# Performance work log

Measured on AMD Instinct MI355X. Metric: run time of the kernel, lower is better.

Reference implementation:

```python
import jax, jax.numpy as jnp
import numpy as np

B = 65536      # batch (edges/nodes)
A = 8          # number of attribute node types (len(cfg.node_types))
E = 128        # embedding_size


def setup_inputs() -> dict:
    key = jax.random.key(0)
    k1, k2, k3, k4, k5 = jax.random.split(key, 5)
    image_features = jax.random.normal(k1, (B, E), dtype=jnp.float32)
    edge_attributes = jax.random.normal(k2, (B, A, E), dtype=jnp.float32)
    # nn.Linear(2E -> E): weight [E, 2E], bias [E]
    W_agg = jax.random.normal(k3, (E, 2 * E), dtype=jnp.float32) * (1.0 / np.sqrt(2 * E))
    b_agg = jax.random.normal(k4, (E,), dtype=jnp.float32) * 0.01
    # per-node-type edge-space projection [A, E, E] (kaiming-uniform-like scale)
    proj = jax.random.uniform(k5, (A, E, E), dtype=jnp.float32, minval=-1.0, maxval=1.0) * np.sqrt(6.0 / E)
    return {
        "image_features": image_features,
        "edge_attributes": edge_attributes,
        "W_agg": W_agg,
        "b_agg": b_agg,
        "proj": proj,
    }


def reference(image_features, edge_attributes, W_agg, b_agg, proj):
    # src_embeddings.unsqueeze(1).repeat(1, A, 1) -> broadcast, no copy
    src = jnp.broadcast_to(image_features[:, None, :], edge_attributes.shape)  # [B, A, E]
    x = jnp.concatenate([src, edge_attributes], axis=-1)                       # [B, A, 2E]
    agg = jnp.einsum('bak,ik->bai', x, W_agg) + b_agg                          # Linear(2E->E)
    out = jnp.einsum('bai,aij->baj', agg, proj)                                # per-type matmul
    return out
```

## Files before the change

kernel.cpp:

```cpp
#include <hip/hip_runtime.h>
#include <hip/hip_bf16.h>

typedef __attribute__((ext_vector_type(8))) short short8;
typedef __attribute__((ext_vector_type(4))) float floatx4;

__device__ inline short f2bf(float f) {
  unsigned u = __builtin_bit_cast(unsigned, f);
  unsigned r = u + 0x7fffu + ((u >> 16) & 1u);
  return (short)(r >> 16);
}

__device__ inline short8 cvt8(float4 a, float4 b) {
  short8 r;
  r[0] = f2bf(a.x); r[1] = f2bf(a.y); r[2] = f2bf(a.z); r[3] = f2bf(a.w);
  r[4] = f2bf(b.x); r[5] = f2bf(b.y); r[6] = f2bf(b.z); r[7] = f2bf(b.w);
  return r;
}

__global__ __launch_bounds__(256) void prep_M(
    const float* __restrict__ W, const float* __restrict__ proj,
    const float* __restrict__ bvec, short* __restrict__ Mt,
    float* __restrict__ bias2) {
  int blk = blockIdx.x;
  int a = blk >> 7, j = blk & 127;
  int k = threadIdx.x;
  const float* pj = proj + a * 16384 + j;
  float acc = 0.f;
#pragma unroll 4
  for (int i = 0; i < 128; ++i)
    acc += W[i * 256 + k] * pj[i * 128];
  Mt[a * 32768 + j * 256 + k] = f2bf(acc);
  if (k == 0) {
    float b = 0.f;
    for (int i = 0; i < 128; ++i) b += bvec[i] * pj[i * 128];
    bias2[a * 128 + j] = b;
  }
}

__global__ __launch_bounds__(256) void gemm_main(
    const float* __restrict__ img, const float* __restrict__ edge,
    const short* __restrict__ Mt, const float* __restrict__ bias2,
    float* __restrict__ out) {
  constexpr int LDA = 40;
  __shared__ short As[128 * LDA];
  __shared__ short Bs[128 * LDA];

  const int tid = threadIdx.x;
  const int a = blockIdx.x & 7;
  const int b0 = (blockIdx.x >> 3) << 7;
  const int wave = tid >> 6, lane = tid & 63;
  const int quad = lane >> 4, l16 = lane & 15;
  const int wm = wave & 1, wn = wave >> 1;

  floatx4 acc[4][4] = {};
  const short* Mta = Mt + a * 32768;

  for (int ks = 0; ks < 8; ++ks) {
#pragma unroll
    for (int i = 0; i < 2; ++i) {
      int slot = tid + i * 256;
      int row = slot >> 2, c8 = slot & 3;
      const float* src;
      if (ks < 4)
        src = img + (size_t)(b0 + row) * 128 + ks * 32 + c8 * 8;
      else
        src = edge + (size_t)(b0 + row) * 1024 + a * 128 + (ks - 4) * 32 + c8 * 8;
      float4 v0 = *(const float4*)src;
      float4 v1 = *(const float4*)(src + 4);
      *(short8*)&As[row * LDA + c8 * 8] = cvt8(v0, v1);
    }
#pragma unroll
    for (int i = 0; i < 2; ++i) {
      int chunk = tid + i * 256;
      int row = chunk >> 2, c = chunk & 3;
      *(short8*)&Bs[row * LDA + c * 8] =
          *(const short8*)(Mta + row * 256 + ks * 32 + c * 8);
    }
    __syncthreads();

    short8 af[4], bfr[4];
#pragma unroll
    for (int mt = 0; mt < 4; ++mt)
      af[mt] = *(const short8*)&As[(wm * 64 + mt * 16 + l16) * LDA + quad * 8];
#pragma unroll
    for (int nt = 0; nt < 4; ++nt)
      bfr[nt] = *(const short8*)&Bs[(wn * 64 + nt * 16 + l16) * LDA + quad * 8];
#pragma unroll
    for (int mt = 0; mt < 4; ++mt)
#pragma unroll
      for (int nt = 0; nt < 4; ++nt)
        acc[mt][nt] = __builtin_amdgcn_mfma_f32_16x16x32_bf16(
            af[mt], bfr[nt], acc[mt][nt], 0, 0, 0);
    __syncthreads();
  }

  float bias[4];
#pragma unroll
  for (int nt = 0; nt < 4; ++nt)
    bias[nt] = bias2[a * 128 + wn * 64 + nt * 16 + l16];
#pragma unroll
  for (int mt = 0; mt < 4; ++mt)
#pragma unroll
    for (int nt = 0; nt < 4; ++nt) {
      int j = wn * 64 + nt * 16 + l16;
#pragma unroll
      for (int r = 0; r < 4; ++r) {
        int b = b0 + wm * 64 + mt * 16 + quad * 4 + r;
        out[(size_t)b * 1024 + a * 128 + j] = acc[mt][nt][r] + bias[nt];
      }
    }
}

extern "C" void kernel_launch(void* const* d_in, const int* in_sizes, int n_in,
                              void* d_out, int out_size, void* d_ws,
                              size_t ws_size, hipStream_t stream) {
  const float* img  = (const float*)d_in[0];
  const float* edge = (const float*)d_in[1];
  const float* W    = (const float*)d_in[2];
  const float* bv   = (const float*)d_in[3];
  const float* proj = (const float*)d_in[4];
  float* out = (float*)d_out;

  short* Mt = (short*)d_ws;
  float* bias2 = (float*)((char*)d_ws + 8 * 128 * 256 * 2);

  prep_M<<<1024, 256, 0, stream>>>(W, proj, bv, Mt, bias2);
  gemm_main<<<4096, 256, 0, stream>>>(img, edge, Mt, bias2, out);
}
```

Before: 508.5 us.

## Load MFMA fragments directly from global memory, dropping LDS staging and barriers

```diff
diff --git a/kernel.cpp b/kernel.cpp
--- a/kernel.cpp
+++ b/kernel.cpp
@@ -37,14 +37,10 @@
   }
 }
 
-__global__ __launch_bounds__(256) void gemm_main(
+__global__ __launch_bounds__(256, 3) void gemm_main(
     const float* __restrict__ img, const float* __restrict__ edge,
     const short* __restrict__ Mt, const float* __restrict__ bias2,
     float* __restrict__ out) {
-  constexpr int LDA = 40;
-  __shared__ short As[128 * LDA];
-  __shared__ short Bs[128 * LDA];
-
   const int tid = threadIdx.x;
   const int a = blockIdx.x & 7;
   const int b0 = (blockIdx.x >> 3) << 7;
@@ -53,45 +49,46 @@
   const int wm = wave & 1, wn = wave >> 1;
 
   floatx4 acc[4][4] = {};
+
+  const float* imgB[4];
+  const float* edgeB[4];
+  const short* mB[4];
+#pragma unroll
+  for (int mt = 0; mt < 4; ++mt) {
+    int row = b0 + wm * 64 + mt * 16 + l16;
+    imgB[mt]  = img  + (size_t)row * 128  + quad * 8;
+    edgeB[mt] = edge + (size_t)row * 1024 + a * 128 + quad * 8;
+  }
   const short* Mta = Mt + a * 32768;
+#pragma unroll
+  for (int nt = 0; nt < 4; ++nt)
+    mB[nt] = Mta + (wn * 64 + nt * 16 + l16) * 256 + quad * 8;
 
+#pragma unroll
   for (int ks = 0; ks < 8; ++ks) {
+    float4 v0[4], v1[4];
+    short8 bfr[4];
 #pragma unroll
-    for (int i = 0; i < 2; ++i) {
-      int slot = tid + i * 256;
-      int row = slot >> 2, c8 = slot & 3;
-      const float* src;
-      if (ks < 4)
-        src = img + (size_t)(b0 + row) * 128 + ks * 32 + c8 * 8;
-      else
-        src = edge + (size_t)(b0 + row) * 1024 + a * 128 + (ks - 4) * 32 + c8 * 8;
-      float4 v0 = *(const float4*)src;
-      float4 v1 = *(const float4*)(src + 4);
-      *(short8*)&As[row * LDA + c8 * 8] = cvt8(v0, v1);
+    for (int mt = 0; mt < 4; ++mt) {
+      const float* s = (ks < 4) ? (imgB[mt] + ks * 32)
+                                : (edgeB[mt] + (ks - 4) * 32);
+      v0[mt] = *(const float4*)s;
+      v1[mt] = *(const float4*)(s + 4);
     }
 #pragma unroll
-    for (int i = 0; i < 2; ++i) {
-      int chunk = tid + i * 256;
-      int row = chunk >> 2, c = chunk & 3;
-      *(short8*)&Bs[row * LDA + c * 8] =
-          *(const short8*)(Mta + row * 256 + ks * 32 + c * 8);
-    }
-    __syncthreads();
+    for (int nt = 0; nt < 4; ++nt)
+      bfr[nt] = *(const short8*)(mB[nt] + ks * 32);
 
-    short8 af[4], bfr[4];
+    short8 af[4];
 #pragma unroll
-    for (int mt = 0; mt < 4; ++mt)
-      af[mt] = *(const short8*)&As[(wm * 64 + mt * 16 + l16) * LDA + quad * 8];
-#pragma unroll
-    for (int nt = 0; nt < 4; ++nt)
-      bfr[nt] = *(const short8*)&Bs[(wn * 64 + nt * 16 + l16) * LDA + quad * 8];
+    for (int mt = 0; mt < 4; ++mt) af[mt] = cvt8(v0[mt], v1[mt]);
+
 #pragma unroll
     for (int mt = 0; mt < 4; ++mt)
 #pragma unroll
       for (int nt = 0; nt < 4; ++nt)
         acc[mt][nt] = __builtin_amdgcn_mfma_f32_16x16x32_bf16(
             af[mt], bfr[nt], acc[mt][nt], 0, 0, 0);
-    __syncthreads();
   }
 
   float bias[4];
```

Measured after the change: 615.8 us. 1.21x slower.

## Restructure GEMM to 16-row tiles covering all types, B read from global

Applied to the files above, without the earlier changes.

```diff
diff --git a/kernel.cpp b/kernel.cpp
--- a/kernel.cpp
+++ b/kernel.cpp
@@ -1,7 +1,7 @@
 #include <hip/hip_runtime.h>
-#include <hip/hip_bf16.h>
 
 typedef __attribute__((ext_vector_type(8))) short short8;
+typedef __attribute__((ext_vector_type(4))) short bfx4;
 typedef __attribute__((ext_vector_type(4))) float floatx4;
 
 __device__ inline short f2bf(float f) {
@@ -10,10 +10,9 @@
   return (short)(r >> 16);
 }
 
-__device__ inline short8 cvt8(float4 a, float4 b) {
-  short8 r;
+__device__ inline bfx4 cvt4(float4 a) {
+  bfx4 r;
   r[0] = f2bf(a.x); r[1] = f2bf(a.y); r[2] = f2bf(a.z); r[3] = f2bf(a.w);
-  r[4] = f2bf(b.x); r[5] = f2bf(b.y); r[6] = f2bf(b.z); r[7] = f2bf(b.w);
   return r;
 }
 
@@ -29,7 +28,9 @@
 #pragma unroll 4
   for (int i = 0; i < 128; ++i)
     acc += W[i * 256 + k] * pj[i * 128];
-  Mt[a * 32768 + j * 256 + k] = f2bf(acc);
+  int ks = k >> 5, quad = (k >> 3) & 3, e = k & 7;
+  int nt = j >> 4, l16 = j & 15;
+  Mt[((a * 8 + ks) * 8 + nt) * 512 + l16 * 32 + quad * 8 + e] = f2bf(acc);
   if (k == 0) {
     float b = 0.f;
     for (int i = 0; i < 128; ++i) b += bvec[i] * pj[i * 128];
@@ -37,78 +38,60 @@
   }
 }
 
-__global__ __launch_bounds__(256) void gemm_main(
+__global__ __launch_bounds__(512, 4) void gemm_main(
     const float* __restrict__ img, const float* __restrict__ edge,
     const short* __restrict__ Mt, const float* __restrict__ bias2,
     float* __restrict__ out) {
-  constexpr int LDA = 40;
-  __shared__ short As[128 * LDA];
-  __shared__ short Bs[128 * LDA];
+  __shared__ short imgS[16 * 136];
+  __shared__ short edgeS[16 * 1032];
 
   const int tid = threadIdx.x;
-  const int a = blockIdx.x & 7;
-  const int b0 = (blockIdx.x >> 3) << 7;
-  const int wave = tid >> 6, lane = tid & 63;
+  const int b0 = blockIdx.x << 4;
+  const int wave = tid >> 6;
+  const int lane = tid & 63;
   const int quad = lane >> 4, l16 = lane & 15;
-  const int wm = wave & 1, wn = wave >> 1;
 
-  floatx4 acc[4][4] = {};
-  const short* Mta = Mt + a * 32768;
+  float4 vi = *(const float4*)(img + (size_t)(b0 + (tid >> 5)) * 128 + (tid & 31) * 4);
+  float4 ve[8];
+#pragma unroll
+  for (int i = 0; i < 8; ++i) {
+    int f = i * 512 + tid;
+    ve[i] = *(const float4*)(edge + (size_t)(b0 + (f >> 8)) * 1024 + (f & 255) * 4);
+  }
+  *(bfx4*)((char*)imgS + (tid >> 5) * 272 + (tid & 31) * 8) = cvt4(vi);
+#pragma unroll
+  for (int i = 0; i < 8; ++i) {
+    int f = i * 512 + tid;
+    *(bfx4*)((char*)edgeS + (f >> 8) * 2064 + (f & 255) * 8) = cvt4(ve[i]);
+  }
+  __syncthreads();
 
+  const short* mB = Mt + wave * 32768 + l16 * 32 + quad * 8;
+  floatx4 acc[8] = {};
+#pragma unroll
   for (int ks = 0; ks < 8; ++ks) {
+    short8 af;
+    if (ks < 4)
+      af = *(const short8*)((const char*)imgS + l16 * 272 + (ks * 32 + quad * 8) * 2);
+    else
+      af = *(const short8*)((const char*)edgeS +
+                            l16 * 2064 + (wave * 128 + (ks - 4) * 32 + quad * 8) * 2);
 #pragma unroll
-    for (int i = 0; i < 2; ++i) {
-      int slot = tid + i * 256;
-      int row = slot >> 2, c8 = slot & 3;
-      const float* src;
-      if (ks < 4)
-        src = img + (size_t)(b0 + row) * 128 + ks * 32 + c8 * 8;
-      else
-        src = edge + (size_t)(b0 + row) * 1024 + a * 128 + (ks - 4) * 32 + c8 * 8;
-      float4 v0 = *(const float4*)src;
-      float4 v1 = *(const float4*)(src + 4);
-      *(short8*)&As[row * LDA + c8 * 8] = cvt8(v0, v1);
+    for (int nt = 0; nt < 8; ++nt) {
+      short8 bf = *(const short8*)(mB + ks * 4096 + nt * 512);
+      acc[nt] = __builtin_amdgcn_mfma_f32_16x16x32_bf16(af, bf, acc[nt], 0, 0, 0);
     }
-#pragma unroll
-    for (int i = 0; i < 2; ++i) {
-      int chunk = tid + i * 256;
-      int row = chunk >> 2, c = chunk & 3;
-      *(short8*)&Bs[row * LDA + c * 8] =
-          *(const short8*)(Mta + row * 256 + ks * 32 + c * 8);
-    }
-    __syncthreads();
-
-    short8 af[4], bfr[4];
-#pragma unroll
-    for (int mt = 0; mt < 4; ++mt)
-      af[mt] = *(const short8*)&As[(wm * 64 + mt * 16 + l16) * LDA + quad * 8];
-#pragma unroll
-    for (int nt = 0; nt < 4; ++nt)
-      bfr[nt] = *(const short8*)&Bs[(wn * 64 + nt * 16 + l16) * LDA + quad * 8];
-#pragma unroll
-    for (int mt = 0; mt < 4; ++mt)
-#pragma unroll
-      for (int nt = 0; nt < 4; ++nt)
-        acc[mt][nt] = __builtin_amdgcn_mfma_f32_16x16x32_bf16(
-            af[mt], bfr[nt], acc[mt][nt], 0, 0, 0);
-    __syncthreads();
   }
 
-  float bias[4];
+  float bias[8];
 #pragma unroll
-  for (int nt = 0; nt < 4; ++nt)
-    bias[nt] = bias2[a * 128 + wn * 64 + nt * 16 + l16];
+  for (int nt = 0; nt < 8; ++nt) bias[nt] = bias2[wave * 128 + nt * 16 + l16];
+  float* ob = out + (size_t)b0 * 1024 + wave * 128 + l16;
 #pragma unroll
-  for (int mt = 0; mt < 4; ++mt)
+  for (int nt = 0; nt < 8; ++nt)
 #pragma unroll
-    for (int nt = 0; nt < 4; ++nt) {
-      int j = wn * 64 + nt * 16 + l16;
-#pragma unroll
-      for (int r = 0; r < 4; ++r) {
-        int b = b0 + wm * 64 + mt * 16 + quad * 4 + r;
-        out[(size_t)b * 1024 + a * 128 + j] = acc[mt][nt][r] + bias[nt];
-      }
-    }
+    for (int r = 0; r < 4; ++r)
+      ob[(size_t)(quad * 4 + r) * 1024 + nt * 16] = acc[nt][r] + bias[nt];
 }
 
 extern "C" void kernel_launch(void* const* d_in, const int* in_sizes, int n_in,
@@ -125,5 +108,5 @@
   float* bias2 = (float*)((char*)d_ws + 8 * 128 * 256 * 2);
 
   prep_M<<<1024, 256, 0, stream>>>(W, proj, bv, Mt, bias2);
-  gemm_main<<<4096, 256, 0, stream>>>(img, edge, Mt, bias2, out);
+  gemm_main<<<4096, 512, 0, stream>>>(img, edge, Mt, bias2, out);
 }
```

Measured after the change: 560.2 us. +10.2%, slower.
